# Performance work log

Measured on AMD Instinct MI355X. Metric: run time of the kernel, lower is better.

Reference implementation:

```python
import jax, jax.numpy as jnp
import numpy as np

H = 1024
M = 4096
K = 64            # max_memory_updates_per_step
THRESH = 0.5      # surprise_threshold
EPS = 1e-12


def setup_inputs() -> dict:
    key = jax.random.key(0)
    ks = jax.random.split(key, 5)
    B, S = 4, 2048
    return {
        "hidden_states": jax.random.normal(ks[0], (B, S, H), dtype=jnp.float32),
        "ln_gamma": jnp.ones((H,), jnp.float32),
        "ln_beta": jnp.zeros((H,), jnp.float32),
        "Wq": jax.random.normal(ks[1], (H, H), jnp.float32) * 0.02,
        "bq": jnp.zeros((H,), jnp.float32),
        "Wo": jax.random.normal(ks[2], (H, H), jnp.float32) * 0.02,
        "bo": jnp.zeros((H,), jnp.float32),
        "memory": jax.random.normal(ks[3], (M, H), jnp.float32),
        "importance_scores": jax.random.uniform(ks[4], (M,), jnp.float32),
    }


def _layer_norm(x, g, b):
    mu = jnp.mean(x, axis=-1, keepdims=True)
    var = jnp.mean(jnp.square(x - mu), axis=-1, keepdims=True)
    return (x - mu) * jax.lax.rsqrt(var + EPS) * g + b


def reference(hidden_states, ln_gamma, ln_beta, Wq, bq, Wo, bo, memory, importance_scores):
    # LayerNorm
    norm = _layer_norm(hidden_states, ln_gamma, ln_beta)  # [B,S,H]

    # Surprise measure (detached): mean |x| over hidden dim
    surprise = jnp.mean(jnp.abs(jax.lax.stop_gradient(norm)), axis=-1)  # [B,S]

    # --- surprise-based memory update (buffers; no gradient, training mode) ---
    flat_h = jax.lax.stop_gradient(norm).reshape(-1, H)   # [B*S, H]
    flat_s = surprise.reshape(-1)                          # [B*S]
    # top-K surprises, descending (matches where>thr -> sort desc -> take K)
    top_vals, top_idx = jax.lax.top_k(flat_s, K)
    valid = top_vals > THRESH                              # entries below threshold: no write
    # K slots with smallest importance, ascending importance order
    _, slots = jax.lax.top_k(-importance_scores, K)
    new_rows = flat_h[top_idx]                             # [K, H]
    old_rows = memory[slots]                               # [K, H]
    mem = memory.at[slots].set(jnp.where(valid[:, None], new_rows, old_rows))  # [M,H]

    # --- query memory ---
    q = jnp.einsum("bsh,oh->bso", norm, Wq) + bq           # query_proj
    sim = jnp.einsum("bsh,mh->bsm", q, mem)                # [B,S,M]
    attn = jax.nn.softmax(sim, axis=-1)
    retrieved = jnp.einsum("bsm,mh->bsh", attn, mem)       # [B,S,H]
    mem_out = jnp.einsum("bsh,oh->bso", retrieved, Wo) + bo  # output_proj

    # dropout in eval mode = identity; residual add
    return hidden_states + mem_out
```

## Files before the change

### kernel.cpp

```cpp
#include <hip/hip_runtime.h>

#define H 1024
#define MMEM 4096
#define NTOK 8192
#define KTOP 64
#define FTHRESH 0.5f

typedef _Float16 half8 __attribute__((ext_vector_type(8)));
typedef float vf4 __attribute__((ext_vector_type(4)));

__device__ __forceinline__ short f2h(float x){
  union { _Float16 h; short s; } u; u.h = (_Float16)x; return u.s;
}
__device__ __forceinline__ float h2f(short s){
  union { _Float16 h; short s; } u; u.s = s; return (float)u.h;
}
__device__ __forceinline__ unsigned fkey_of(float x){
  unsigned u = __float_as_uint(x);
  return (u & 0x80000000u) ? ~u : (u | 0x80000000u);
}
__device__ __forceinline__ float val_of(unsigned k){
  unsigned u = (k & 0x80000000u) ? (k & 0x7fffffffu) : ~k;
  return __uint_as_float(u);
}

__device__ __forceinline__ void gload_lds16(const short* g, short* l){
  __builtin_amdgcn_global_load_lds(
      (const __attribute__((address_space(1))) unsigned int*)g,
      (__attribute__((address_space(3))) unsigned int*)l, 16, 0, 0);
}

__global__ __launch_bounds__(256) void ln_prep_kernel(
    const float* __restrict__ hs, const float* __restrict__ g, const float* __restrict__ be,
    const float* __restrict__ mem, const float* __restrict__ Wq, const float* __restrict__ Wo,
    const float* __restrict__ bq,
    short* __restrict__ n16, float* __restrict__ surprise,
    short* __restrict__ m16, short* __restrict__ wqT, short* __restrict__ wo16,
    float* __restrict__ biasM)
{
  int b = blockIdx.x, tid = threadIdx.x;
  if (b < NTOK){
    int row = b;
    long base = (long)row * H;
    float4 x = ((const float4*)(hs + base))[tid];
    float s1 = x.x + x.y + x.z + x.w;
    float s2 = x.x*x.x + x.y*x.y + x.z*x.z + x.w*x.w;
    __shared__ float r1[4], r2[4], r3[4];
    int w = tid >> 6, lane = tid & 63;
    for (int o = 32; o; o >>= 1){ s1 += __shfl_down(s1, o); s2 += __shfl_down(s2, o); }
    if (lane == 0){ r1[w] = s1; r2[w] = s2; }
    __syncthreads();
    float S1 = r1[0]+r1[1]+r1[2]+r1[3];
    float S2 = r2[0]+r2[1]+r2[2]+r2[3];
    float mean = S1 * (1.0f/H);
    float var  = S2 * (1.0f/H) - mean*mean;
    float rinv = rsqrtf(var + 1e-12f);
    float4 gg = ((const float4*)g)[tid];
    float4 bb = ((const float4*)be)[tid];
    float4 n;
    n.x = (x.x-mean)*rinv*gg.x + bb.x;
    n.y = (x.y-mean)*rinv*gg.y + bb.y;
    n.z = (x.z-mean)*rinv*gg.z + bb.z;
    n.w = (x.w-mean)*rinv*gg.w + bb.w;
    float sa = fabsf(n.x)+fabsf(n.y)+fabsf(n.z)+fabsf(n.w);
    for (int o = 32; o; o >>= 1) sa += __shfl_down(sa, o);
    if (lane == 0) r3[w] = sa;
    __syncthreads();
    if (tid == 0) surprise[row] = (r3[0]+r3[1]+r3[2]+r3[3]) * (1.0f/H);
    short4 h4;
    h4.x = f2h(n.x); h4.y = f2h(n.y); h4.z = f2h(n.z); h4.w = f2h(n.w);
    ((short4*)(n16 + base))[tid] = h4;
  } else if (b < NTOK + 4096){
    int mrow = b - NTOK;
    long i = (long)mrow * 256 + tid;
    float4 x = ((const float4*)mem)[i];
    short4 h;
    h.x = f2h(x.x); h.y = f2h(x.y); h.z = f2h(x.z); h.w = f2h(x.w);
    ((short4*)m16)[i] = h;
    float4 b4 = ((const float4*)bq)[tid];
    float sb = b4.x*h2f(h.x) + b4.y*h2f(h.y) + b4.z*h2f(h.z) + b4.w*h2f(h.w);
    int wv = tid >> 6, lane = tid & 63;
    for (int o = 32; o; o >>= 1) sb += __shfl_down(sb, o);
    __shared__ float rb_[4];
    if (lane == 0) rb_[wv] = sb;
    __syncthreads();
    if (tid == 0) biasM[mrow] = rb_[0]+rb_[1]+rb_[2]+rb_[3];
  } else if (b < NTOK + 5120){
    long i = (long)(b - NTOK - 4096) * 256 + tid;
    float4 x = ((const float4*)Wo)[i];
    short4 h;
    h.x = f2h(x.x); h.y = f2h(x.y); h.z = f2h(x.z); h.w = f2h(x.w);
    ((short4*)wo16)[i] = h;
  } else {
    __shared__ __align__(16) short t[64][66];
    int tb = b - NTOK - 5120;
    int r0 = (tb >> 4) * 64, c0 = (tb & 15) * 64;
    #pragma unroll
    for (int k = 0; k < 4; ++k){
      int idx = k*256 + tid;
      int r = idx >> 4, c4 = (idx & 15) * 4;
      float4 x = *(const float4*)&Wq[(long)(r0+r)*H + c0 + c4];
      t[r][c4]   = f2h(x.x);
      t[r][c4+1] = f2h(x.y);
      t[r][c4+2] = f2h(x.z);
      t[r][c4+3] = f2h(x.w);
    }
    __syncthreads();
    #pragma unroll
    for (int k = 0; k < 4; ++k){
      int idx = k*256 + tid;
      int c = idx >> 4, r4 = (idx & 15) * 4;
      short4 h;
      h.x = t[r4][c]; h.y = t[r4+1][c]; h.z = t[r4+2][c]; h.w = t[r4+3][c];
      *(short4*)&wqT[(long)(c0+c)*H + r0 + r4] = h;
    }
  }
}

__global__ __launch_bounds__(256) void topk_local(
    const float* __restrict__ surprise, const float* __restrict__ imp,
    unsigned long long* __restrict__ cand_s, unsigned long long* __restrict__ cand_i)
{
  __shared__ unsigned long long s[256];
  int b = blockIdx.x, tid = threadIdx.x;
  int maxmode = (b < 32);
  int gidx = maxmode ? (b*256 + tid) : ((b-32)*256 + tid);
  float x = maxmode ? surprise[gidx] : imp[gidx];
  unsigned k = fkey_of(x);
  if (!maxmode) k = ~k;
  s[tid] = ((unsigned long long)k << 32) | (unsigned)(8191 - gidx);
  __syncthreads();
  for (int kk = 2; kk <= 256; kk <<= 1)
    for (int j = kk >> 1; j > 0; j >>= 1){
      int i = tid, ixj = i ^ j;
      if (ixj > i){
        bool asc = ((i & kk) == 0);
        unsigned long long a = s[i], c = s[ixj];
        if ((a < c) == asc){ s[i] = c; s[ixj] = a; }
      }
      __syncthreads();
    }
  if (tid < 64){
    if (maxmode) cand_s[b*64 + tid] = s[tid];
    else         cand_i[(b-32)*64 + tid] = s[tid];
  }
}

__global__ __launch_bounds__(256) void topk_merge(
    const unsigned long long* __restrict__ cand_s, const unsigned long long* __restrict__ cand_i,
    float* __restrict__ top_vals, int* __restrict__ top_idx, int* __restrict__ slots)
{
  __shared__ unsigned long long s[2048];
  int tid = threadIdx.x;
  int N = (blockIdx.x == 0) ? 2048 : 1024;
  const unsigned long long* src = (blockIdx.x == 0) ? cand_s : cand_i;
  for (int i = tid; i < N; i += 256) s[i] = src[i];
  __syncthreads();
  for (int kk = 2; kk <= N; kk <<= 1)
    for (int j = kk >> 1; j > 0; j >>= 1){
      for (int i = tid; i < N; i += 256){
        int ixj = i ^ j;
        if (ixj > i){
          bool asc = ((i & kk) == 0);
          unsigned long long a = s[i], c = s[ixj];
          if ((a < c) == asc){ s[i] = c; s[ixj] = a; }
        }
      }
      __syncthreads();
    }
  if (tid < 64){
    unsigned long long p = s[tid];
    int gi = 8191 - (int)(p & 0xffffffffu);
    if (blockIdx.x == 0){
      top_vals[tid] = val_of((unsigned)(p >> 32));
      top_idx[tid] = gi;
    } else {
      slots[tid] = gi;
    }
  }
}

__global__ __launch_bounds__(256) void update_kernel(
    const float* __restrict__ top_vals, const int* __restrict__ top_idx, const int* __restrict__ slots,
    const float* __restrict__ hs, const float* __restrict__ g, const float* __restrict__ be,
    const float* __restrict__ bq,
    short* __restrict__ m16, float* __restrict__ biasM)
{
  int i = blockIdx.x;
  if (top_vals[i] <= FTHRESH) return;
  int s = slots[i], r = top_idx[i];
  int tid = threadIdx.x, w = tid >> 6, lane = tid & 63;
  long base = (long)r * H;
  float4 x = ((const float4*)(hs + base))[tid];
  float s1 = x.x + x.y + x.z + x.w;
  float s2 = x.x*x.x + x.y*x.y + x.z*x.z + x.w*x.w;
  __shared__ float r1[4], r2[4], rb[4];
  for (int o = 32; o; o >>= 1){ s1 += __shfl_down(s1, o); s2 += __shfl_down(s2, o); }
  if (lane == 0){ r1[w] = s1; r2[w] = s2; }
  __syncthreads();
  float S1 = r1[0]+r1[1]+r1[2]+r1[3];
  float S2 = r2[0]+r2[1]+r2[2]+r2[3];
  float mean = S1 * (1.0f/H);
  float var  = S2 * (1.0f/H) - mean*mean;
  float rinv = rsqrtf(var + 1e-12f);
  float4 gg = ((const float4*)g)[tid];
  float4 bb = ((const float4*)be)[tid];
  short4 h4;
  h4.x = f2h((x.x-mean)*rinv*gg.x + bb.x);
  h4.y = f2h((x.y-mean)*rinv*gg.y + bb.y);
  h4.z = f2h((x.z-mean)*rinv*gg.z + bb.z);
  h4.w = f2h((x.w-mean)*rinv*gg.w + bb.w);
  ((short4*)(m16 + (long)s*H))[tid] = h4;
  float4 b4 = ((const float4*)bq)[tid];
  float sb = b4.x*h2f(h4.x) + b4.y*h2f(h4.y) + b4.z*h2f(h4.z) + b4.w*h2f(h4.w);
  for (int o = 32; o; o >>= 1) sb += __shfl_down(sb, o);
  if (lane == 0) rb[w] = sb;
  __syncthreads();
  if (tid == 0) biasM[s] = rb[0]+rb[1]+rb[2]+rb[3];
}

__global__ __launch_bounds__(256) void gemm_dual(
    const short* __restrict__ A0, const short* __restrict__ B0, int N0, short* __restrict__ O0,
    const short* __restrict__ A1, const short* __restrict__ B1, int N1, short* __restrict__ O1,
    int K)
{
  __shared__ short sA[128*64];
  __shared__ short sB[128*64];
  int tid = threadIdx.x, w = tid >> 6, lane = tid & 63, ln = lane & 15, quad = lane >> 4;
  int wr = w >> 1, wc = w & 1;
  int lin = blockIdx.x;
  int nl  = (lin & 7) * 64 + (lin >> 3);
  int second = (nl >= 256);
  int t = second ? (nl - 256) : nl;
  const short* A = second ? A1 : A0;
  const short* B = second ? B1 : B0;
  short* O = second ? O1 : O0;
  int N = second ? N1 : N0;
  int nwgx = N >> 7;
  long m0 = (long)(t / nwgx) * 128, n0 = (long)(t % nwgx) * 128;
  long Kl = K;
  vf4 acc[4][4];
  #pragma unroll
  for (int i = 0; i < 4; ++i) for (int j = 0; j < 4; ++j) for (int r = 0; r < 4; ++r) acc[i][j][r] = 0.0f;

  for (long kk = 0; kk < Kl; kk += 64){
    #pragma unroll
    for (int j = 0; j < 4; ++j){
      int f = (w*4 + j)*64 + lane;
      int row = f >> 3, c8 = f & 7;
      long go = kk + (long)((c8 ^ (row & 7)) * 8);
      gload_lds16(A + (m0+row)*Kl + go, sA + (w*4+j)*512);
      gload_lds16(B + (n0+row)*Kl + go, sB + (w*4+j)*512);
    }
    __syncthreads();
    #pragma unroll
    for (int ks = 0; ks < 64; ks += 32){
      int cbase = (ks >> 3) + quad;
      half8 bh[4];
      #pragma unroll
      for (int j = 0; j < 4; ++j){
        int rb = wc*64 + j*16 + ln;
        bh[j] = *(const half8*)&sB[rb*64 + (cbase ^ (rb & 7))*8];
      }
      #pragma unroll
      for (int i = 0; i < 4; ++i){
        int ra = wr*64 + i*16 + ln;
        half8 a = *(const half8*)&sA[ra*64 + (cbase ^ (ra & 7))*8];
        #pragma unroll
        for (int j = 0; j < 4; ++j)
          acc[i][j] = __builtin_amdgcn_mfma_f32_16x16x32_f16(a, bh[j], acc[i][j], 0, 0, 0);
      }
    }
    __syncthreads();
  }

  #pragma unroll
  for (int i = 0; i < 4; ++i)
    #pragma unroll
    for (int j = 0; j < 4; ++j)
      #pragma unroll
      for (int r = 0; r < 4; ++r){
        long row = m0 + wr*64 + i*16 + quad*4 + r;
        long col = n0 + wc*64 + j*16 + ln;
        O[row*(long)N + col] = f2h(acc[i][j][r]);
      }
}

template<int MODE>
__global__ __launch_bounds__(512, 2) void gemm256(
    const short* __restrict__ A, const short* __restrict__ B,
    int K, int N,
    short* __restrict__ O1, float* __restrict__ Of,
    const float* __restrict__ resid, const float* __restrict__ biasN)
{
  extern __shared__ short lds[];
  int tid = threadIdx.x, w = tid >> 6, lane = tid & 63, ln = lane & 15, quad = lane >> 4;
  int wr = w >> 2, wc = w & 3;
  int nwgx = gridDim.x;
  int lin = blockIdx.y * nwgx + blockIdx.x;
  int xcd = lin & 7, ii = lin >> 3;
  int mt = (xcd >> 1)*8 + (ii >> 3);
  int nt = (xcd & 1)*8 + (ii & 7);
  long m0 = (long)mt * 256, n0 = (long)nt * 256;
  long Kl = K;
  int NT = K >> 6;

  auto STAGE = [&](const short* __restrict__ G, long rowbase, long kt, short* ldsbase){
    #pragma unroll
    for (int i = 0; i < 2; ++i){
      int f = i*512 + tid;
      int row = f >> 3, c8 = f & 7;
      long go = kt + (long)((c8 ^ (row & 7)) * 8);
      gload_lds16(G + (rowbase + row)*Kl + go, ldsbase + i*4096 + w*512);
    }
  };
  auto LOADA = [&](half8 (&af)[4][2], const short* sAh){
    #pragma unroll
    for (int ks = 0; ks < 2; ++ks){
      int cbase = ks*4 + quad;
      #pragma unroll
      for (int i = 0; i < 4; ++i){
        int ra = wr*64 + i*16 + ln;
        af[i][ks] = *(const half8*)&sAh[ra*64 + (cbase ^ (ra & 7))*8];
      }
    }
  };
  auto LOADB = [&](half8 (&bf)[2][2], const short* sBh){
    #pragma unroll
    for (int ks = 0; ks < 2; ++ks){
      int cbase = ks*4 + quad;
      #pragma unroll
      for (int j = 0; j < 2; ++j){
        int rb = wc*32 + j*16 + ln;
        bf[j][ks] = *(const half8*)&sBh[rb*64 + (cbase ^ (rb & 7))*8];
      }
    }
  };

  vf4 acc[4][4][2];
  #pragma unroll
  for (int p = 0; p < 4; ++p)
    for (int i = 0; i < 4; ++i)
      for (int j = 0; j < 2; ++j)
        for (int r = 0; r < 4; ++r) acc[p][i][j][r] = 0.0f;

  {
    int t1 = (NT > 1) ? 1 : 0;
    STAGE(A, m0 + 0,   0, lds + 0);
    STAGE(B, n0 + 0,   0, lds + 16384);
    STAGE(B, n0 + 128, 0, lds + 16384 + 8192);
    STAGE(A, m0 + 128, 0, lds + 8192);
    STAGE(A, m0 + 0,   (long)t1*64, lds + 32768);
    STAGE(B, n0 + 0,   (long)t1*64, lds + 32768 + 16384);
  }
  asm volatile("s_waitcnt vmcnt(8)" ::: "memory");
  asm volatile("s_barrier" ::: "memory");

  #define PH_MID()  do { \
    asm volatile("s_waitcnt lgkmcnt(0)" ::: "memory"); \
    __builtin_amdgcn_sched_barrier(0); \
    __builtin_amdgcn_s_setprio(1); } while(0)
  #define PH_END() do { \
    __builtin_amdgcn_s_setprio(0); \
    asm volatile("s_waitcnt vmcnt(8)" ::: "memory"); \
    asm volatile("s_barrier" ::: "memory"); } while(0)
  #define MFMA16(ap, af, bf) do { \
    _Pragma("unroll") \
    for (int i = 0; i < 4; ++i){ \
      _Pragma("unroll") \
      for (int j = 0; j < 2; ++j){ \
        ap[i][j] = __builtin_amdgcn_mfma_f32_16x16x32_f16(af[i][0], bf[j][0], ap[i][j], 0, 0, 0); \
        ap[i][j] = __builtin_amdgcn_mfma_f32_16x16x32_f16(af[i][1], bf[j][1], ap[i][j], 0, 0, 0); \
      } \
    } } while(0)

  for (int t = 0; t < NT; ++t){
    int cur = t & 1;
    short* bA = lds + cur*32768;
    short* bB = bA + 16384;
    short* oA = lds + (cur^1)*32768;
    short* oB = oA + 16384;
    int t1 = t + 1; if (t1 >= NT) t1 -= NT;
    int t2 = t + 2; if (t2 >= NT) t2 -= NT;
    long kt1 = (long)t1 * 64, kt2 = (long)t2 * 64;
    half8 af[4][2], bf0[2][2], bf1[2][2];

    LOADA(af, bA);
    LOADB(bf0, bB);
    STAGE(B, n0 + 128, kt1, oB + 8192);
    PH_MID();
    MFMA16(acc[0], af, bf0);
    PH_END();

    LOADB(bf1, bB + 8192);
    STAGE(A, m0 + 128, kt1, oA + 8192);
    PH_MID();
    MFMA16(acc[1], af, bf1);
    PH_END();

    LOADA(af, bA + 8192);
    STAGE(A, m0 + 0, kt2, bA);
    PH_MID();
    MFMA16(acc[2], af, bf0);
    PH_END();

    STAGE(B, n0 + 0, kt2, bB);
    PH_MID();
    MFMA16(acc[3], af, bf1);
    PH_END();
  }
  #undef PH_MID
  #undef PH_END
  #undef MFMA16

  float bn[2][2];
  if (MODE != 2){
    #pragma unroll
    for (int bh = 0; bh < 2; ++bh)
      for (int j = 0; j < 2; ++j)
        bn[bh][j] = biasN[n0 + bh*128 + wc*32 + j*16 + ln];
  }
  #pragma unroll
  for (int p = 0; p < 4; ++p){
    #pragma unroll
    for (int i = 0; i < 4; ++i){
      #pragma unroll
      for (int j = 0; j < 2; ++j){
        #pragma unroll
        for (int r = 0; r < 4; ++r){
          long row = m0 + (p >> 1)*128 + wr*64 + i*16 + quad*4 + r;
          long col = n0 + (p & 1)*128 + wc*32 + j*16 + ln;
          float v = acc[p][i][j][r];
          if (MODE == 1){
            O1[row*(long)N + col] = f2h(v + bn[p & 1][j]);
          } else if (MODE == 2){
            O1[row*(long)N + col] = f2h(v);
          } else {
            Of[row*(long)N + col] = v + resid[row*(long)N + col] + bn[p & 1][j];
          }
        }
      }
    }
  }
}

__global__ __launch_bounds__(512, 2) void gemm_out(
    const short* __restrict__ A, const short* __restrict__ B,
    int K, int N,
    float* __restrict__ Of, const float* __restrict__ resid, const float* __restrict__ biasN)
{
  extern __shared__ short lds[];
  int tid = threadIdx.x, w = tid >> 6, lane = tid & 63, ln = lane & 15, quad = lane >> 4;
  int wr = (w >> 2) & 1, wc = w & 3;
  int nwgx = gridDim.x, nwg = nwgx * gridDim.y;
  int lin = blockIdx.y * nwgx + blockIdx.x;
  int nl  = (lin & 7) * (nwg >> 3) + (lin >> 3);
  long m0 = (long)(nl >> 2) * 128, n0 = (long)(nl & 3) * 256;
  long Kl = K;
  int NT = K >> 6;

  auto STAGE_A = [&](long rowbase, long kt, short* dst){
    int f = tid;
    int row = f >> 3, c8 = f & 7;
    long go = kt + (long)((c8 ^ (row & 7)) * 8);
    gload_lds16(A + (rowbase + row)*Kl + go, dst + w*512);
  };
  auto STAGE_B = [&](long rowbase, long kt, short* dst){
    #pragma unroll
    for (int i = 0; i < 2; ++i){
      int f = i*512 + tid;
      int row = f >> 3, c8 = f & 7;
      long go = kt + (long)((c8 ^ (row & 7)) * 8);
      gload_lds16(B + (rowbase + row)*Kl + go, dst + i*4096 + w*512);
    }
  };
  auto LOADA = [&](half8 (&af)[2][2], const short* sAh){
    #pragma unroll
    for (int ks = 0; ks < 2; ++ks){
      int cbase = ks*4 + quad;
      #pragma unroll
      for (int i = 0; i < 2; ++i){
        int ra = wr*32 + i*16 + ln;
        af[i][ks] = *(const half8*)&sAh[ra*64 + (cbase ^ (ra & 7))*8];
      }
    }
  };
  auto LOADB = [&](half8 (&bf)[2][2], const short* sBh){
    #pragma unroll
    for (int ks = 0; ks < 2; ++ks){
      int cbase = ks*4 + quad;
      #pragma unroll
      for (int j = 0; j < 2; ++j){
        int rb = wc*32 + j*16 + ln;
        bf[j][ks] = *(const half8*)&sBh[rb*64 + (cbase ^ (rb & 7))*8];
      }
    }
  };

  vf4 acc[4][2][2];
  #pragma unroll
  for (int p = 0; p < 4; ++p)
    for (int i = 0; i < 2; ++i)
      for (int j = 0; j < 2; ++j)
        for (int r = 0; r < 4; ++r) acc[p][i][j][r] = 0.0f;

  {
    int t1 = (NT > 1) ? 1 : 0;
    STAGE_A(m0 + 0,   0, lds + 0);
    STAGE_B(n0 + 0,   0, lds + 8192);
    STAGE_B(n0 + 128, 0, lds + 16384);
    STAGE_A(m0 + 64,  0, lds + 4096);
    STAGE_A(m0 + 0,   (long)t1*64, lds + 24576);
    STAGE_B(n0 + 0,   (long)t1*64, lds + 24576+8192);
  }
  asm volatile("s_waitcnt vmcnt(6)" ::: "memory");
  asm volatile("s_barrier" ::: "memory");

  #define FPH_MID()  do { \
    asm volatile("s_waitcnt lgkmcnt(0)" ::: "memory"); \
    __builtin_amdgcn_sched_barrier(0); \
    __builtin_amdgcn_s_setprio(1); } while(0)
  #define FPH_END() do { \
    __builtin_amdgcn_s_setprio(0); \
    asm volatile("s_waitcnt vmcnt(6)" ::: "memory"); \
    asm volatile("s_barrier" ::: "memory"); } while(0)
  #define MFMA8(ap, af, bf) do { \
    _Pragma("unroll") \
    for (int i = 0; i < 2; ++i){ \
      _Pragma("unroll") \
      for (int j = 0; j < 2; ++j){ \
        ap[i][j] = __builtin_amdgcn_mfma_f32_16x16x32_f16(af[i][0], bf[j][0], ap[i][j], 0, 0, 0); \
        ap[i][j] = __builtin_amdgcn_mfma_f32_16x16x32_f16(af[i][1], bf[j][1], ap[i][j], 0, 0, 0); \
      } \
    } } while(0)

  for (int t = 0; t < NT; ++t){
    int cur = t & 1;
    short* bA = lds + cur*24576;
    short* oA = lds + (cur^1)*24576;
    int t1 = t + 1; if (t1 >= NT) t1 -= NT;
    int t2 = t + 2; if (t2 >= NT) t2 -= NT;
    long kt1 = (long)t1 * 64, kt2 = (long)t2 * 64;
    half8 af[2][2], bf0[2][2], bf1[2][2];

    LOADA(af, bA);
    LOADB(bf0, bA + 8192);
    STAGE_B(n0 + 128, kt1, oA + 16384);
    FPH_MID();
    MFMA8(acc[0], af, bf0);
    FPH_END();

    LOADB(bf1, bA + 16384);
    STAGE_A(m0 + 64, kt1, oA + 4096);
    FPH_MID();
    MFMA8(acc[1], af, bf1);
    FPH_END();

    LOADA(af, bA + 4096);
    STAGE_A(m0 + 0, kt2, bA);
    FPH_MID();
    MFMA8(acc[2], af, bf0);
    FPH_END();

    STAGE_B(n0 + 0, kt2, bA + 8192);
    FPH_MID();
    MFMA8(acc[3], af, bf1);
    FPH_END();
  }
  #undef FPH_MID
  #undef FPH_END
  #undef MFMA8

  float bn[2][2];
  #pragma unroll
  for (int bh = 0; bh < 2; ++bh)
    for (int j = 0; j < 2; ++j)
      bn[bh][j] = biasN[n0 + bh*128 + wc*32 + j*16 + ln];
  #pragma unroll
  for (int p = 0; p < 4; ++p){
    #pragma unroll
    for (int i = 0; i < 2; ++i){
      #pragma unroll
      for (int j = 0; j < 2; ++j){
        #pragma unroll
        for (int r = 0; r < 4; ++r){
          long row = m0 + (p >> 1)*64 + wr*32 + i*16 + quad*4 + r;
          long col = n0 + (p & 1)*128 + wc*32 + j*16 + ln;
          Of[row*(long)N + col] = acc[p][i][j][r] + resid[row*(long)N + col] + bn[p & 1][j];
        }
      }
    }
  }
}

__global__ __launch_bounds__(256) void softmax_kernel(short* __restrict__ simP)
{
  long row = blockIdx.x;
  int tid = threadIdx.x, w = tid >> 6, lane = tid & 63;
  half8* ptr = (half8*)(simP + row*MMEM);
  float xf[16];
  float mx = -1e30f;
  #pragma unroll
  for (int j = 0; j < 2; ++j){
    half8 x = ptr[tid + j*256];
    #pragma unroll
    for (int e = 0; e < 8; ++e){ float f = (float)x[e]; xf[j*8+e] = f; mx = fmaxf(mx, f); }
  }
  for (int o = 32; o; o >>= 1) mx = fmaxf(mx, __shfl_xor(mx, o));
  __shared__ float rmax[4], rsum[4];
  if (lane == 0) rmax[w] = mx;
  __syncthreads();
  mx = fmaxf(fmaxf(rmax[0], rmax[1]), fmaxf(rmax[2], rmax[3]));
  float p[16], s = 0.f;
  #pragma unroll
  for (int k = 0; k < 16; ++k){ p[k] = __expf(xf[k] - mx); s += p[k]; }
  for (int o = 32; o; o >>= 1) s += __shfl_xor(s, o);
  if (lane == 0) rsum[w] = s;
  __syncthreads();
  float inv = 1.0f / (rsum[0]+rsum[1]+rsum[2]+rsum[3]);
  #pragma unroll
  for (int j = 0; j < 2; ++j){
    half8 o8;
    #pragma unroll
    for (int e = 0; e < 8; ++e) o8[e] = (_Float16)(p[j*8+e] * inv);
    ptr[tid + j*256] = o8;
  }
}

extern "C" void kernel_launch(void* const* d_in, const int* in_sizes, int n_in,
                              void* d_out, int out_size, void* d_ws, size_t ws_size,
                              hipStream_t stream)
{
  const float* hs  = (const float*)d_in[0];
  const float* gam = (const float*)d_in[1];
  const float* bet = (const float*)d_in[2];
  const float* Wq  = (const float*)d_in[3];
  const float* bq  = (const float*)d_in[4];
  const float* Wo  = (const float*)d_in[5];
  const float* bo  = (const float*)d_in[6];
  const float* mem = (const float*)d_in[7];
  const float* imp = (const float*)d_in[8];
  float* out = (float*)d_out;

  char* ws = (char*)d_ws;
  short* n16   = (short*)(ws);
  short* g16   = (short*)(ws + (16ull<<20));
  short* m16   = (short*)(ws + (32ull<<20));
  short* wqT   = (short*)(ws + (40ull<<20));
  short* simP  = (short*)(ws + (48ull<<20));
  short* vwoT  = (short*)(ws + (112ull<<20));
  short* wo16  = (short*)(ws + (132ull<<20));
  char*  tail  = ws + (134ull<<20);
  float* biasM    = (float*)tail;
  float* surprise = (float*)(tail + (64<<10));
  float* top_vals = (float*)(tail + (128<<10));
  int*   top_idx  = (int*)  (tail + (129<<10));
  int*   slots    = (int*)  (tail + (130<<10));
  unsigned long long* cand_s = (unsigned long long*)(tail + (132<<10));
  unsigned long long* cand_i = (unsigned long long*)(tail + (148<<10));

  static bool attr_done = false;
  if (!attr_done){
    (void)hipFuncSetAttribute(reinterpret_cast<const void*>(&gemm256<1>),
                              hipFuncAttributeMaxDynamicSharedMemorySize, 131072);
    (void)hipFuncSetAttribute(reinterpret_cast<const void*>(&gemm_out),
                              hipFuncAttributeMaxDynamicSharedMemorySize, 98304);
    attr_done = true;
  }

  ln_prep_kernel<<<NTOK + 5376, 256, 0, stream>>>(
      hs, gam, bet, mem, Wq, Wo, bq, n16, surprise, m16, wqT, wo16, biasM);
  topk_local<<<48, 256, 0, stream>>>(surprise, imp, cand_s, cand_i);
  topk_merge<<<2, 256, 0, stream>>>(cand_s, cand_i, top_vals, top_idx, slots);
  update_kernel<<<KTOP, 256, 0, stream>>>(top_vals, top_idx, slots, hs, gam, bet, bq, m16, biasM);
  gemm_dual<<<512, 256, 0, stream>>>(
      wo16, m16, MMEM, vwoT,  m16, wqT, H, g16,  H);
  gemm256<1><<<dim3(16,32), 512, 131072, stream>>>(
      n16, g16, H, MMEM, simP, nullptr, nullptr, biasM);
  softmax_kernel<<<NTOK, 256, 0, stream>>>(simP);
  gemm_out<<<dim3(4, 64), 512, 98304, stream>>>(
      simP, vwoT, MMEM, H, out, hs, bo);
}
```

Measured before the change: 367.2 us.

## Fuse softmax into output GEMM with per-row max/sum prologue and deferred normalization

Drops the separate softmax kernel. The output GEMM now computes each row's max and exp-sum in a prologue that reads its 128 logit rows. It then applies exp(x - max) to the A fragments before the MFMAs and scales by 1/sum in the epilogue. This removes one full read and write of the 8192x4096 fp16 score matrix. The cost is that each of the 4 column blocks re-reads its rows in the prologue and recomputes exp, so exp and logit reads are repeated fourfold.

```diff
diff --git a/kernel.cpp b/kernel.cpp
--- a/kernel.cpp
+++ b/kernel.cpp
@@ -450,6 +450,7 @@
     float* __restrict__ Of, const float* __restrict__ resid, const float* __restrict__ biasN)
 {
   extern __shared__ short lds[];
+  __shared__ float mrow[128], invz[128];
   int tid = threadIdx.x, w = tid >> 6, lane = tid & 63, ln = lane & 15, quad = lane >> 4;
   int wr = (w >> 2) & 1, wc = w & 3;
   int nwgx = gridDim.x, nwg = nwgx * gridDim.y;
@@ -459,6 +460,34 @@
   long Kl = K;
   int NT = K >> 6;
 
+  for (int rr = 0; rr < 16; ++rr){
+    int row = w*16 + rr;
+    const half8* rp = (const half8*)(A + (m0 + row)*Kl);
+    half8 v[8];
+    #pragma unroll
+    for (int c = 0; c < 8; ++c) v[c] = rp[lane + c*64];
+    float mx = -1e30f;
+    #pragma unroll
+    for (int c = 0; c < 8; ++c)
+      #pragma unroll
+      for (int e = 0; e < 8; ++e) mx = fmaxf(mx, (float)v[c][e]);
+    for (int o = 32; o; o >>= 1) mx = fmaxf(mx, __shfl_xor(mx, o));
+    float s = 0.f;
+    #pragma unroll
+    for (int c = 0; c < 8; ++c)
+      #pragma unroll
+      for (int e = 0; e < 8; ++e) s += __expf((float)v[c][e] - mx);
+    for (int o = 32; o; o >>= 1) s += __shfl_xor(s, o);
+    if (lane == 0){ mrow[row] = mx; invz[row] = 1.0f / s; }
+  }
+  __syncthreads();
+
+  float mv[2][2];
+  #pragma unroll
+  for (int h = 0; h < 2; ++h)
+    for (int i = 0; i < 2; ++i)
+      mv[h][i] = mrow[h*64 + wr*32 + i*16 + ln];
+
   auto STAGE_A = [&](long rowbase, long kt, short* dst){
     int f = tid;
     int row = f >> 3, c8 = f & 7;
@@ -524,6 +553,18 @@
     __builtin_amdgcn_s_setprio(0); \
     asm volatile("s_waitcnt vmcnt(6)" ::: "memory"); \
     asm volatile("s_barrier" ::: "memory"); } while(0)
+  #define EXPA(af, h) do { \
+    _Pragma("unroll") \
+    for (int i = 0; i < 2; ++i){ \
+      _Pragma("unroll") \
+      for (int ks = 0; ks < 2; ++ks){ \
+        _Pragma("unroll") \
+        for (int e = 0; e < 8; ++e){ \
+          float f_ = (float)af[i][ks][e]; \
+          af[i][ks][e] = (_Float16)__expf(f_ - mv[h][i]); \
+        } \
+      } \
+    } } while(0)
   #define MFMA8(ap, af, bf) do { \
     _Pragma("unroll") \
     for (int i = 0; i < 2; ++i){ \
@@ -547,6 +588,7 @@
     LOADB(bf0, bA + 8192);
     STAGE_B(n0 + 128, kt1, oA + 16384);
     FPH_MID();
+    EXPA(af, 0);
     MFMA8(acc[0], af, bf0);
     FPH_END();
 
@@ -559,6 +601,7 @@
     LOADA(af, bA + 4096);
     STAGE_A(m0 + 0, kt2, bA);
     FPH_MID();
+    EXPA(af, 1);
     MFMA8(acc[2], af, bf0);
     FPH_END();
 
@@ -569,6 +612,7 @@
   }
   #undef FPH_MID
   #undef FPH_END
+  #undef EXPA
   #undef MFMA8
 
   float bn[2][2];
@@ -584,46 +628,13 @@
       for (int j = 0; j < 2; ++j){
         #pragma unroll
         for (int r = 0; r < 4; ++r){
-          long row = m0 + (p >> 1)*64 + wr*32 + i*16 + quad*4 + r;
+          int lr = (p >> 1)*64 + wr*32 + i*16 + quad*4 + r;
+          long row = m0 + lr;
           long col = n0 + (p & 1)*128 + wc*32 + j*16 + ln;
-          Of[row*(long)N + col] = acc[p][i][j][r] + resid[row*(long)N + col] + bn[p & 1][j];
+          Of[row*(long)N + col] = acc[p][i][j][r]*invz[lr] + resid[row*(long)N + col] + bn[p & 1][j];
         }
       }
     }
-  }
-}
-
-__global__ __launch_bounds__(256) void softmax_kernel(short* __restrict__ simP)
-{
-  long row = blockIdx.x;
-  int tid = threadIdx.x, w = tid >> 6, lane = tid & 63;
-  half8* ptr = (half8*)(simP + row*MMEM);
-  float xf[16];
-  float mx = -1e30f;
-  #pragma unroll
-  for (int j = 0; j < 2; ++j){
-    half8 x = ptr[tid + j*256];
-    #pragma unroll
-    for (int e = 0; e < 8; ++e){ float f = (float)x[e]; xf[j*8+e] = f; mx = fmaxf(mx, f); }
-  }
-  for (int o = 32; o; o >>= 1) mx = fmaxf(mx, __shfl_xor(mx, o));
-  __shared__ float rmax[4], rsum[4];
-  if (lane == 0) rmax[w] = mx;
-  __syncthreads();
-  mx = fmaxf(fmaxf(rmax[0], rmax[1]), fmaxf(rmax[2], rmax[3]));
-  float p[16], s = 0.f;
-  #pragma unroll
-  for (int k = 0; k < 16; ++k){ p[k] = __expf(xf[k] - mx); s += p[k]; }
-  for (int o = 32; o; o >>= 1) s += __shfl_xor(s, o);
-  if (lane == 0) rsum[w] = s;
-  __syncthreads();
-  float inv = 1.0f / (rsum[0]+rsum[1]+rsum[2]+rsum[3]);
-  #pragma unroll
-  for (int j = 0; j < 2; ++j){
-    half8 o8;
-    #pragma unroll
-    for (int e = 0; e < 8; ++e) o8[e] = (_Float16)(p[j*8+e] * inv);
-    ptr[tid + j*256] = o8;
   }
 }
 
@@ -677,7 +688,6 @@
       wo16, m16, MMEM, vwoT,  m16, wqT, H, g16,  H);
   gemm256<1><<<dim3(16,32), 512, 131072, stream>>>(
       n16, g16, H, MMEM, simP, nullptr, nullptr, biasM);
-  softmax_kernel<<<NTOK, 256, 0, stream>>>(simP);
   gemm_out<<<dim3(4, 64), 512, 98304, stream>>>(
       simP, vwoT, MMEM, H, out, hs, bo);
 }
```

New measurement: 456.2 us. 1.24x slower.

## Rewrite dual precompute GEMM with 128x256 tiles and pipelined LDS prefetch

Applied to the files above, without the earlier changes.

Replaces the 128x128-tile gemm_dual (256 threads, static LDS, sync-per-k-step) with gemm_dual2, which uses 512-thread blocks computing 128x256 tiles. Global-to-LDS loads are double-buffered and interleaved between four MFMA phases, with explicit waitcnt and barrier control and raised wave priority during MFMA. It aims to hide memory latency and cut the number of blocks and syncs. The trade is more LDS (96KB) and a more fragile hand-scheduled pipeline.

```diff
diff --git a/kernel.cpp b/kernel.cpp
--- a/kernel.cpp
+++ b/kernel.cpp
@@ -219,71 +219,156 @@
   if (tid == 0) biasM[s] = rb[0]+rb[1]+rb[2]+rb[3];
 }
 
-__global__ __launch_bounds__(256) void gemm_dual(
-    const short* __restrict__ A0, const short* __restrict__ B0, int N0, short* __restrict__ O0,
-    const short* __restrict__ A1, const short* __restrict__ B1, int N1, short* __restrict__ O1,
+__global__ __launch_bounds__(512, 2) void gemm_dual2(
+    const short* __restrict__ A0, const short* __restrict__ B0,
+    const short* __restrict__ A1, const short* __restrict__ B1,
+    short* __restrict__ O0, short* __restrict__ O1v,
     int K)
 {
-  __shared__ short sA[128*64];
-  __shared__ short sB[128*64];
+  extern __shared__ short lds[];
   int tid = threadIdx.x, w = tid >> 6, lane = tid & 63, ln = lane & 15, quad = lane >> 4;
-  int wr = w >> 1, wc = w & 1;
+  int wr = (w >> 2) & 1, wc = w & 3;
   int lin = blockIdx.x;
-  int nl  = (lin & 7) * 64 + (lin >> 3);
-  int second = (nl >= 256);
-  int t = second ? (nl - 256) : nl;
+  int nl  = (lin & 7) * 32 + (lin >> 3);
+  int second = (nl >= 128);
+  int q = second ? (nl - 128) : nl;
   const short* A = second ? A1 : A0;
   const short* B = second ? B1 : B0;
-  short* O = second ? O1 : O0;
-  int N = second ? N1 : N0;
-  int nwgx = N >> 7;
-  long m0 = (long)(t / nwgx) * 128, n0 = (long)(t % nwgx) * 128;
+  short* O = second ? O1v : O0;
+  int N = second ? H : MMEM;
+  long m0, n0;
+  if (second){ m0 = (long)(q >> 2) * 128; n0 = (long)(q & 3) * 256; }
+  else       { m0 = (long)(q >> 4) * 128; n0 = (long)(q & 15) * 256; }
   long Kl = K;
-  vf4 acc[4][4];
-  #pragma unroll
-  for (int i = 0; i < 4; ++i) for (int j = 0; j < 4; ++j) for (int r = 0; r < 4; ++r) acc[i][j][r] = 0.0f;
-
-  for (long kk = 0; kk < Kl; kk += 64){
-    #pragma unroll
-    for (int j = 0; j < 4; ++j){
-      int f = (w*4 + j)*64 + lane;
+  int NT = K >> 6;
+
+  auto STAGE_A = [&](long rowbase, long kt, short* dst){
+    int f = tid;
+    int row = f >> 3, c8 = f & 7;
+    long go = kt + (long)((c8 ^ (row & 7)) * 8);
+    gload_lds16(A + (rowbase + row)*Kl + go, dst + w*512);
+  };
+  auto STAGE_B = [&](long rowbase, long kt, short* dst){
+    #pragma unroll
+    for (int i = 0; i < 2; ++i){
+      int f = i*512 + tid;
       int row = f >> 3, c8 = f & 7;
-      long go = kk + (long)((c8 ^ (row & 7)) * 8);
-      gload_lds16(A + (m0+row)*Kl + go, sA + (w*4+j)*512);
-      gload_lds16(B + (n0+row)*Kl + go, sB + (w*4+j)*512);
-    }
-    __syncthreads();
-    #pragma unroll
-    for (int ks = 0; ks < 64; ks += 32){
-      int cbase = (ks >> 3) + quad;
-      half8 bh[4];
-      #pragma unroll
-      for (int j = 0; j < 4; ++j){
-        int rb = wc*64 + j*16 + ln;
-        bh[j] = *(const half8*)&sB[rb*64 + (cbase ^ (rb & 7))*8];
-      }
-      #pragma unroll
-      for (int i = 0; i < 4; ++i){
-        int ra = wr*64 + i*16 + ln;
-        half8 a = *(const half8*)&sA[ra*64 + (cbase ^ (ra & 7))*8];
+      long go = kt + (long)((c8 ^ (row & 7)) * 8);
+      gload_lds16(B + (rowbase + row)*Kl + go, dst + i*4096 + w*512);
+    }
+  };
+  auto LOADA = [&](half8 (&af)[2][2], const short* sAh){
+    #pragma unroll
+    for (int ks = 0; ks < 2; ++ks){
+      int cbase = ks*4 + quad;
+      #pragma unroll
+      for (int i = 0; i < 2; ++i){
+        int ra = wr*32 + i*16 + ln;
+        af[i][ks] = *(const half8*)&sAh[ra*64 + (cbase ^ (ra & 7))*8];
+      }
+    }
+  };
+  auto LOADB = [&](half8 (&bf)[2][2], const short* sBh){
+    #pragma unroll
+    for (int ks = 0; ks < 2; ++ks){
+      int cbase = ks*4 + quad;
+      #pragma unroll
+      for (int j = 0; j < 2; ++j){
+        int rb = wc*32 + j*16 + ln;
+        bf[j][ks] = *(const half8*)&sBh[rb*64 + (cbase ^ (rb & 7))*8];
+      }
+    }
+  };
+
+  vf4 acc[4][2][2];
+  #pragma unroll
+  for (int p = 0; p < 4; ++p)
+    for (int i = 0; i < 2; ++i)
+      for (int j = 0; j < 2; ++j)
+        for (int r = 0; r < 4; ++r) acc[p][i][j][r] = 0.0f;
+
+  {
+    int t1 = (NT > 1) ? 1 : 0;
+    STAGE_A(m0 + 0,   0, lds + 0);
+    STAGE_B(n0 + 0,   0, lds + 8192);
+    STAGE_B(n0 + 128, 0, lds + 16384);
+    STAGE_A(m0 + 64,  0, lds + 4096);
+    STAGE_A(m0 + 0,   (long)t1*64, lds + 24576);
+    STAGE_B(n0 + 0,   (long)t1*64, lds + 24576+8192);
+  }
+  asm volatile("s_waitcnt vmcnt(6)" ::: "memory");
+  asm volatile("s_barrier" ::: "memory");
+
+  #define DPH_MID()  do { \
+    asm volatile("s_waitcnt lgkmcnt(0)" ::: "memory"); \
+    __builtin_amdgcn_sched_barrier(0); \
+    __builtin_amdgcn_s_setprio(1); } while(0)
+  #define DPH_END() do { \
+    __builtin_amdgcn_s_setprio(0); \
+    asm volatile("s_waitcnt vmcnt(6)" ::: "memory"); \
+    asm volatile("s_barrier" ::: "memory"); } while(0)
+  #define DMFMA8(ap, af, bf) do { \
+    _Pragma("unroll") \
+    for (int i = 0; i < 2; ++i){ \
+      _Pragma("unroll") \
+      for (int j = 0; j < 2; ++j){ \
+        ap[i][j] = __builtin_amdgcn_mfma_f32_16x16x32_f16(af[i][0], bf[j][0], ap[i][j], 0, 0, 0); \
+        ap[i][j] = __builtin_amdgcn_mfma_f32_16x16x32_f16(af[i][1], bf[j][1], ap[i][j], 0, 0, 0); \
+      } \
+    } } while(0)
+
+  for (int t = 0; t < NT; ++t){
+    int cur = t & 1;
+    short* bA = lds + cur*24576;
+    short* oA = lds + (cur^1)*24576;
+    int t1 = t + 1; if (t1 >= NT) t1 -= NT;
+    int t2 = t + 2; if (t2 >= NT) t2 -= NT;
+    long kt1 = (long)t1 * 64, kt2 = (long)t2 * 64;
+    half8 af[2][2], bf0[2][2], bf1[2][2];
+
+    LOADA(af, bA);
+    LOADB(bf0, bA + 8192);
+    STAGE_B(n0 + 128, kt1, oA + 16384);
+    DPH_MID();
+    DMFMA8(acc[0], af, bf0);
+    DPH_END();
+
+    LOADB(bf1, bA + 16384);
+    STAGE_A(m0 + 64, kt1, oA + 4096);
+    DPH_MID();
+    DMFMA8(acc[1], af, bf1);
+    DPH_END();
+
+    LOADA(af, bA + 4096);
+    STAGE_A(m0 + 0, kt2, bA);
+    DPH_MID();
+    DMFMA8(acc[2], af, bf0);
+    DPH_END();
+
+    STAGE_B(n0 + 0, kt2, bA + 8192);
+    DPH_MID();
+    DMFMA8(acc[3], af, bf1);
+    DPH_END();
+  }
+  #undef DPH_MID
+  #undef DPH_END
+  #undef DMFMA8
+
+  #pragma unroll
+  for (int p = 0; p < 4; ++p){
+    #pragma unroll
+    for (int i = 0; i < 2; ++i){
+      #pragma unroll
+      for (int j = 0; j < 2; ++j){
         #pragma unroll
-        for (int j = 0; j < 4; ++j)
-          acc[i][j] = __builtin_amdgcn_mfma_f32_16x16x32_f16(a, bh[j], acc[i][j], 0, 0, 0);
-      }
-    }
-    __syncthreads();
-  }
-
-  #pragma unroll
-  for (int i = 0; i < 4; ++i)
-    #pragma unroll
-    for (int j = 0; j < 4; ++j)
-      #pragma unroll
-      for (int r = 0; r < 4; ++r){
-        long row = m0 + wr*64 + i*16 + quad*4 + r;
-        long col = n0 + wc*64 + j*16 + ln;
-        O[row*(long)N + col] = f2h(acc[i][j][r]);
-      }
+        for (int r = 0; r < 4; ++r){
+          long row = m0 + (p >> 1)*64 + wr*32 + i*16 + quad*4 + r;
+          long col = n0 + (p & 1)*128 + wc*32 + j*16 + ln;
+          O[row*(long)N + col] = f2h(acc[p][i][j][r]);
+        }
+      }
+    }
+  }
 }
 
 template<int MODE>
@@ -665,6 +750,8 @@
                               hipFuncAttributeMaxDynamicSharedMemorySize, 131072);
     (void)hipFuncSetAttribute(reinterpret_cast<const void*>(&gemm_out),
                               hipFuncAttributeMaxDynamicSharedMemorySize, 98304);
+    (void)hipFuncSetAttribute(reinterpret_cast<const void*>(&gemm_dual2),
+                              hipFuncAttributeMaxDynamicSharedMemorySize, 98304);
     attr_done = true;
   }
 
@@ -673,8 +760,8 @@
   topk_local<<<48, 256, 0, stream>>>(surprise, imp, cand_s, cand_i);
   topk_merge<<<2, 256, 0, stream>>>(cand_s, cand_i, top_vals, top_idx, slots);
   update_kernel<<<KTOP, 256, 0, stream>>>(top_vals, top_idx, slots, hs, gam, bet, bq, m16, biasM);
-  gemm_dual<<<512, 256, 0, stream>>>(
-      wo16, m16, MMEM, vwoT,  m16, wqT, H, g16,  H);
+  gemm_dual2<<<256, 512, 98304, stream>>>(
+      wo16, m16, m16, wqT, vwoT, g16, H);
   gemm256<1><<<dim3(16,32), 512, 131072, stream>>>(
       n16, g16, H, MMEM, simP, nullptr, nullptr, biasM);
   softmax_kernel<<<NTOK, 256, 0, stream>>>(simP);
```

New measurement: 363.2 us. Within noise of the previous version (-1.1%).
